# Kernel tuning notes

Measured on AMD Instinct MI355X. Metric: run time of the kernel, lower is better.

## Reference

```python
import jax, jax.numpy as jnp
import numpy as np

N, F_NODE, DIM, H, K, OUT, L = 200000, 16, 3, 128, 20, 4, 4


def setup_inputs() -> dict:
    key = jax.random.key(0)
    ks = jax.random.split(key, 10)
    x = jax.random.normal(ks[0], (N, F_NODE), jnp.float32)
    pos = jax.random.normal(ks[1], (N, DIM), jnp.float32)
    y = jax.random.normal(ks[2], (DIM,), jnp.float32)
    # eigenvector-like basis, roughly orthonormal columns scale
    phi = jax.random.normal(ks[3], (N, K), jnp.float32) / np.sqrt(N).astype(np.float32)
    # torch Linear convention: W is [out, in], y = x @ W.T + b
    lift_w = jax.random.normal(ks[4], (H, F_NODE + 2 * DIM), jnp.float32) * 0.05
    lift_b = jnp.zeros((H,), jnp.float32)
    lin_w = jax.random.normal(ks[5], (L, H, H), jnp.float32) * 0.05  # per-layer, bias=False
    kernel = jax.random.normal(ks[6], (L, K, H, H), jnp.float32) * 0.05
    lower_w = jax.random.normal(ks[7], (OUT, H), jnp.float32) * 0.05
    lower_b = jnp.zeros((OUT,), jnp.float32)
    return dict(x=x, pos=pos, y=y, phi=phi, lift_w=lift_w, lift_b=lift_b,
                lin_w=lin_w, kernel=kernel, lower_w=lower_w, lower_b=lower_b)


def reference(x, pos, y, phi, lift_w, lift_b, lin_w, kernel, lower_w, lower_b):
    # lift: concat node feats, positions, broadcast global y -> [N, F_NODE+2*DIM]
    h = jnp.concatenate([x, pos, y * jnp.ones_like(pos)], axis=1) @ lift_w.T + lift_b
    # pinv(phi) is identical every layer in the original; compute once. [K, N]
    phi_pinv = jnp.linalg.pinv(phi)
    for l in range(L):
        v = phi_pinv @ h                              # [K, H] spectral coefficients
        rv = jnp.einsum('kij,kj->ki', kernel[l], v)   # batched mode matvec (= nested vmap)
        h = jax.nn.elu(h @ lin_w[l].T + phi @ rv)     # [N, H]
    return h @ lower_w.T + lower_b                    # [N, OUT]
```

## Files before the change

kernel.cpp:

```cpp
#include <hip/hip_runtime.h>
#include <math.h>

#define Nn 200000
#define NT 3125

typedef __attribute__((ext_vector_type(8))) short short8;
typedef __attribute__((ext_vector_type(16))) float floatx16;

#define SWZ4(row, g) (((g) ^ ((row) & 7)) << 2)

__device__ __forceinline__ unsigned rnbf(float x) {
    unsigned u = __builtin_bit_cast(unsigned, x);
    return (u + 0x7fffu + ((u >> 16) & 1u)) >> 16;
}
__device__ __forceinline__ float asf(unsigned u) { return __builtin_bit_cast(float, u); }
__device__ __forceinline__ unsigned packf(float x) {
    unsigned hb = rnbf(x);
    float fh = asf(hb << 16);
    unsigned lb = rnbf(x - fh);
    return hb | (lb << 16);
}
__device__ __forceinline__ void permsplit(const unsigned* e, short8& hi, short8& lo) {
    uint4 h, l;
    h.x = __builtin_amdgcn_perm(e[1], e[0], 0x05040100u);
    h.y = __builtin_amdgcn_perm(e[3], e[2], 0x05040100u);
    h.z = __builtin_amdgcn_perm(e[5], e[4], 0x05040100u);
    h.w = __builtin_amdgcn_perm(e[7], e[6], 0x05040100u);
    l.x = __builtin_amdgcn_perm(e[1], e[0], 0x07060302u);
    l.y = __builtin_amdgcn_perm(e[3], e[2], 0x07060302u);
    l.z = __builtin_amdgcn_perm(e[5], e[4], 0x07060302u);
    l.w = __builtin_amdgcn_perm(e[7], e[6], 0x07060302u);
    hi = __builtin_bit_cast(short8, h);
    lo = __builtin_bit_cast(short8, l);
}
__device__ __forceinline__ void permsplit2(uint4 q0, uint4 q1, short8& hi, short8& lo) {
    unsigned e[8] = { q0.x, q0.y, q0.z, q0.w, q1.x, q1.y, q1.z, q1.w };
    permsplit(e, hi, lo);
}

__device__ __forceinline__ void pt_accum(const unsigned* As, const unsigned* Ph,
                                         float* __restrict__ PTc_blk, int t) {
    int lane = t & 63, w = t >> 6;
    int ln = lane & 31, hw = lane >> 5;
    int j0 = w * 32;
    floatx16 ap;
#pragma unroll
    for (int i = 0; i < 16; i++) ap[i] = 0.f;
#pragma unroll
    for (int ks = 0; ks < 4; ks++) {
        unsigned pa[8], e[8];
#pragma unroll
        for (int j = 0; j < 8; j++) {
            int node = ks * 16 + 8 * hw + j;
            pa[j] = Ph[node * 32 + SWZ4(node, ln >> 2) + (ln & 3)];
            int col = j0 + ln;
            e[j] = As[node * 128 + SWZ4(node, col >> 2) + (col & 3)];
        }
        short8 a_hi, a_lo, b_hi, b_lo;
        permsplit(pa, a_hi, a_lo);
        permsplit(e, b_hi, b_lo);
        ap = __builtin_amdgcn_mfma_f32_32x32x16_bf16(a_hi, b_hi, ap, 0, 0, 0);
        ap = __builtin_amdgcn_mfma_f32_32x32x16_bf16(a_lo, b_hi, ap, 0, 0, 0);
        ap = __builtin_amdgcn_mfma_f32_32x32x16_bf16(a_hi, b_lo, ap, 0, 0, 0);
    }
#pragma unroll
    for (int r = 0; r < 16; r++) {
        int mode = (r & 3) + 8 * (r >> 2) + 4 * hw;
        if (mode < 20) unsafeAtomicAdd(&PTc_blk[mode * 128 + j0 + ln], ap[r]);
    }
}

__device__ __forceinline__ void pt_mfma8(const unsigned* As, const unsigned* Ph,
                                         floatx16& ap, int t) {
    int lane = t & 63, w = t >> 6;
    int ln = lane & 31, hw = lane >> 5;
    int j0 = (w & 3) * 32;
    int nh = w >> 2;
#pragma unroll
    for (int i = 0; i < 16; i++) ap[i] = 0.f;
#pragma unroll
    for (int ks2 = 0; ks2 < 2; ks2++) {
        int ks = nh * 2 + ks2;
        unsigned pa[8], e[8];
#pragma unroll
        for (int j = 0; j < 8; j++) {
            int node = ks * 16 + 8 * hw + j;
            pa[j] = Ph[node * 32 + SWZ4(node, ln >> 2) + (ln & 3)];
            int col = j0 + ln;
            e[j] = As[node * 128 + SWZ4(node, col >> 2) + (col & 3)];
        }
        short8 a_hi, a_lo, b_hi, b_lo;
        permsplit(pa, a_hi, a_lo);
        permsplit(e, b_hi, b_lo);
        ap = __builtin_amdgcn_mfma_f32_32x32x16_bf16(a_hi, b_hi, ap, 0, 0, 0);
        ap = __builtin_amdgcn_mfma_f32_32x32x16_bf16(a_lo, b_hi, ap, 0, 0, 0);
        ap = __builtin_amdgcn_mfma_f32_32x32x16_bf16(a_hi, b_lo, ap, 0, 0, 0);
    }
}

__global__ void ptreduce_k(const float* __restrict__ PTc, float* __restrict__ PT) {
    int j = blockIdx.x * 128 + threadIdx.x;
    float s0 = 0.f, s1 = 0.f, s2 = 0.f, s3 = 0.f;
#pragma unroll
    for (int c = 0; c < 64; c += 4) {
        s0 += PTc[(size_t)c * 2560 + j];
        s1 += PTc[(size_t)(c + 1) * 2560 + j];
        s2 += PTc[(size_t)(c + 2) * 2560 + j];
        s3 += PTc[(size_t)(c + 3) * 2560 + j];
    }
    PT[j] = (s0 + s1) + (s2 + s3);
}

__global__ void bias_fold_k(const float* __restrict__ y, const float* __restrict__ lw,
                            const float* __restrict__ lb, float* __restrict__ b2) {
    int j = threadIdx.x;
    float s = lb[j];
#pragma unroll
    for (int d = 0; d < 3; d++) s += y[d] * lw[j * 22 + 19 + d];
    b2[j] = s;
}

__global__ void wsplit_k(const float* __restrict__ lw, const float* __restrict__ low_w,
                         unsigned short* __restrict__ Wh, unsigned short* __restrict__ Wl,
                         unsigned short* __restrict__ LWh, unsigned short* __restrict__ LWl) {
    int i = blockIdx.x * 256 + threadIdx.x;
    float w;
    unsigned short *ph, *pl;
    int idx;
    if (i < 65536) { w = lw[i]; ph = Wh; pl = Wl; idx = i; }
    else           { w = low_w[i - 65536]; ph = LWh; pl = LWl; idx = i - 65536; }
    unsigned hb = rnbf(w);
    float fh = asf(hb << 16);
    unsigned lb = rnbf(w - fh);
    ph[idx] = (unsigned short)hb;
    pl[idx] = (unsigned short)lb;
}

__global__ __launch_bounds__(256) void lift_k(const float* __restrict__ x,
                                              const float* __restrict__ pos,
                                              const float* __restrict__ phi,
                                              const float* __restrict__ lw,
                                              const float* __restrict__ b2,
                                              unsigned* __restrict__ hpk,
                                              float* __restrict__ PTc) {
    __shared__ union {
        struct { float xs[64][21]; float Wc[20][132]; } a;
        unsigned As[64 * 128];
    } sm;
    __shared__ unsigned Ph[64 * 32];
    int t = threadIdx.x;
    int n0 = blockIdx.x * 64;
    {
        int n = t >> 2, f4 = (t & 3) * 4;
        float4 xv = *(const float4*)(x + (size_t)(n0 + n) * 16 + f4);
        sm.a.xs[n][f4 + 0] = xv.x; sm.a.xs[n][f4 + 1] = xv.y;
        sm.a.xs[n][f4 + 2] = xv.z; sm.a.xs[n][f4 + 3] = xv.w;
    }
    if (t < 192) { int n = t / 3, d = t % 3; sm.a.xs[n][16 + d] = pos[(size_t)(n0 + n) * 3 + d]; }
    if (t < 64) sm.a.xs[t][19] = 1.f;
    for (int idx = t; idx < 2560; idx += 256) {
        int k = idx >> 7, j = idx & 127;
        sm.a.Wc[k][j] = (k < 19) ? lw[j * 22 + k] : b2[j];
    }
    for (int idx = t; idx < 2048; idx += 256) {
        int row = idx >> 5, kk = idx & 31;
        float pv = (kk < 20) ? phi[(size_t)(n0 + row) * 20 + kk] : 0.f;
        Ph[row * 32 + SWZ4(row, kk >> 2) + (kk & 3)] = packf(pv);
    }
    __syncthreads();
    int tx = t & 31, ty = t >> 5, i0 = tx * 4;
    float acc[8][4];
#pragma unroll
    for (int m = 0; m < 8; m++)
#pragma unroll
        for (int c = 0; c < 4; c++) acc[m][c] = 0.f;
#pragma unroll 4
    for (int k = 0; k < 20; k++) {
        float4 w = *(const float4*)&sm.a.Wc[k][i0];
#pragma unroll
        for (int m = 0; m < 8; m++) {
            float a = sm.a.xs[ty + 8 * m][k];
            acc[m][0] += a * w.x; acc[m][1] += a * w.y;
            acc[m][2] += a * w.z; acc[m][3] += a * w.w;
        }
    }
    __syncthreads();
#pragma unroll
    for (int m = 0; m < 8; m++) {
        uint4 o;
        o.x = packf(acc[m][0]); o.y = packf(acc[m][1]);
        o.z = packf(acc[m][2]); o.w = packf(acc[m][3]);
        int row = ty + 8 * m;
        *(uint4*)&hpk[(size_t)(n0 + row) * 128 + i0] = o;
        *(uint4*)&sm.As[row * 128 + SWZ4(row, tx)] = o;
    }
    __syncthreads();
    pt_accum(sm.As, Ph, PTc + (size_t)(blockIdx.x & 63) * 2560, t);
}

__global__ void gram_k(const float* __restrict__ phi, float* __restrict__ G) {
    __shared__ float ph[64 * 20];
    int t = threadIdx.x;
    int i0 = t / 20, j0 = t % 20;
    int p1 = t + 256;
    int i1 = p1 / 20, j1 = p1 % 20;
    float a0 = 0.f, a1 = 0.f;
    for (int tile = blockIdx.x; tile < NT; tile += gridDim.x) {
        const float* src = phi + tile * 1280;
        for (int idx = t; idx < 1280; idx += 256) ph[idx] = src[idx];
        __syncthreads();
        for (int n = 0; n < 64; n++) {
            const float* r = ph + n * 20;
            a0 += r[i0] * r[j0];
            if (p1 < 400) a1 += r[i1] * r[j1];
        }
        __syncthreads();
    }
    unsafeAtomicAdd(&G[t], a0);
    if (p1 < 400) unsafeAtomicAdd(&G[p1], a1);
}

__global__ void ginv_k(const float* __restrict__ G, float* __restrict__ Gi) {
    __shared__ float A[20][40];
    __shared__ float colp[20];
    __shared__ float piv;
    int t = threadIdx.x;
    for (int idx = t; idx < 400; idx += 64) {
        int r = idx / 20, c = idx % 20;
        A[r][c] = G[idx];
        A[r][c + 20] = (r == c) ? 1.f : 0.f;
    }
    __syncthreads();
    for (int p = 0; p < 20; p++) {
        if (t == 0) piv = 1.f / A[p][p];
        __syncthreads();
        for (int c = t; c < 40; c += 64) A[p][c] *= piv;
        __syncthreads();
        if (t < 20) colp[t] = A[t][p];
        __syncthreads();
        for (int e = t; e < 800; e += 64) {
            int r = e / 40, c = e % 40;
            if (r != p) A[r][c] -= colp[r] * A[p][c];
        }
        __syncthreads();
    }
    for (int idx = t; idx < 400; idx += 64) {
        int r = idx / 20, c = idx % 20;
        Gi[idx] = A[r][c + 20];
    }
}

__global__ void rv_k(const float* __restrict__ Gi, const float* __restrict__ PT,
                     const float* __restrict__ kern_l,
                     unsigned short* __restrict__ RVh, unsigned short* __restrict__ RVl) {
    __shared__ __align__(16) float v[128];
    __shared__ float part[128];
    int k = blockIdx.x;
    int t = threadIdx.x;
    if (t < 128) {
        const float* gr = Gi + k * 20;
        float s = 0.f;
#pragma unroll
        for (int m = 0; m < 20; m++) s += gr[m] * PT[m * 128 + t];
        v[t] = s;
    }
    __syncthreads();
    int i = t & 127, half = t >> 7;
    const float* kr = kern_l + (size_t)(k * 128 + i) * 128 + half * 64;
    const float* vk = v + half * 64;
    float acc = 0.f;
#pragma unroll 4
    for (int jj = 0; jj < 64; jj += 4) {
        float4 kv = *(const float4*)(kr + jj);
        float4 vv = *(const float4*)(vk + jj);
        acc += kv.x * vv.x + kv.y * vv.y + kv.z * vv.z + kv.w * vv.w;
    }
    if (half) part[i] = acc;
    __syncthreads();
    if (!half) {
        float rv = acc + part[i];
        unsigned hb = rnbf(rv);
        float fh = asf(hb << 16);
        unsigned lb = rnbf(rv - fh);
        RVh[i * 32 + k] = (unsigned short)hb;
        RVl[i * 32 + k] = (unsigned short)lb;
    }
}

__global__ __launch_bounds__(512, 8) void update_k(unsigned* __restrict__ hpk,
                                                   const float* __restrict__ phi,
                                                   const unsigned short* __restrict__ Wh,
                                                   const unsigned short* __restrict__ Wl,
                                                   const unsigned short* __restrict__ RVh,
                                                   const unsigned short* __restrict__ RVl,
                                                   float* __restrict__ ptn,
                                                   const unsigned short* __restrict__ LWh,
                                                   const unsigned short* __restrict__ LWl,
                                                   const float* __restrict__ low_b,
                                                   float* __restrict__ outp) {
    __shared__ __align__(16) unsigned As[64 * 128];
    __shared__ __align__(16) unsigned Ph[64 * 32];
    int t = threadIdx.x;
    int n0 = blockIdx.x * 64;
    for (int idx = t; idx < 2048; idx += 512) {
        int row = idx >> 5, g = idx & 31;
        uint4 v = *(const uint4*)(hpk + (size_t)(n0 + row) * 128 + g * 4);
        *(uint4*)&As[row * 128 + SWZ4(row, g)] = v;
    }
    for (int idx = t; idx < 2048; idx += 512) {
        int row = idx >> 5, kk = idx & 31;
        float pv = (kk < 20) ? phi[(size_t)(n0 + row) * 20 + kk] : 0.f;
        Ph[row * 32 + SWZ4(row, kk >> 2) + (kk & 3)] = packf(pv);
    }
    __syncthreads();

    int lane = t & 63, w = t >> 6;
    int ln = lane & 31, hw = lane >> 5;
    int r0 = (w >> 2) * 32, ct0 = (w & 3) * 32;
    int arow = r0 + ln;

    floatx16 acc;
#pragma unroll
    for (int i = 0; i < 16; i++) acc[i] = 0.f;

    const unsigned short* whp = Wh + (size_t)(ct0 + ln) * 128 + 8 * hw;
    const unsigned short* wlp = Wl + (size_t)(ct0 + ln) * 128 + 8 * hw;
    const unsigned* abase = As + arow * 128;

#pragma unroll
    for (int ks = 0; ks < 8; ks++) {
        int k0 = ks * 16;
        int ga = 4 * ks + 2 * hw;
        uint4 aq0 = *(const uint4*)(abase + SWZ4(arow, ga));
        uint4 aq1 = *(const uint4*)(abase + SWZ4(arow, ga + 1));
        uint4 wh = *(const uint4*)(whp + k0);
        uint4 wl = *(const uint4*)(wlp + k0);
        short8 a_hi, a_lo;
        permsplit2(aq0, aq1, a_hi, a_lo);
        short8 bh = __builtin_bit_cast(short8, wh);
        short8 bl = __builtin_bit_cast(short8, wl);
        acc = __builtin_amdgcn_mfma_f32_32x32x16_bf16(a_hi, bh, acc, 0, 0, 0);
        acc = __builtin_amdgcn_mfma_f32_32x32x16_bf16(a_lo, bh, acc, 0, 0, 0);
        acc = __builtin_amdgcn_mfma_f32_32x32x16_bf16(a_hi, bl, acc, 0, 0, 0);
    }

    const unsigned* pbase = Ph + arow * 32;
#pragma unroll
    for (int ks = 0; ks < 2; ks++) {
        int k0 = ks * 16;
        int gr = 4 * ks + 2 * hw;
        uint4 q0 = *(const uint4*)(pbase + SWZ4(arow, gr));
        uint4 q1 = *(const uint4*)(pbase + SWZ4(arow, gr + 1));
        short8 a_hi, a_lo;
        permsplit2(q0, q1, a_hi, a_lo);
        short8 bh = __builtin_bit_cast(short8, *(const uint4*)(RVh + (size_t)(ct0 + ln) * 32 + k0 + 8 * hw));
        short8 bl = __builtin_bit_cast(short8, *(const uint4*)(RVl + (size_t)(ct0 + ln) * 32 + k0 + 8 * hw));
        acc = __builtin_amdgcn_mfma_f32_32x32x16_bf16(a_hi, bh, acc, 0, 0, 0);
        acc = __builtin_amdgcn_mfma_f32_32x32x16_bf16(a_lo, bh, acc, 0, 0, 0);
        acc = __builtin_amdgcn_mfma_f32_32x32x16_bf16(a_hi, bl, acc, 0, 0, 0);
    }

    unsigned p0[16];
#pragma unroll
    for (int r = 0; r < 16; r++) {
        float v0 = acc[r];
        v0 = v0 > 0.f ? v0 : __expf(v0) - 1.f;
        p0[r] = packf(v0);
    }
    if (!outp) {
#pragma unroll
        for (int r = 0; r < 16; r++) {
            int row = (r & 3) + 8 * (r >> 2) + 4 * hw;
            hpk[(size_t)(n0 + r0 + row) * 128 + ct0 + ln] = p0[r];
        }
    }
    if (ptn || outp) {
        __syncthreads();
#pragma unroll
        for (int r = 0; r < 16; r++) {
            int row = r0 + (r & 3) + 8 * (r >> 2) + 4 * hw;
            int c0 = ct0 + ln;
            As[row * 128 + SWZ4(row, c0 >> 2) + (c0 & 3)] = p0[r];
        }
        __syncthreads();
        if (outp) {
            float* scr = (float*)Ph;
            int r0o = (w >> 1) * 32, kh = w & 1;
            int arow2 = r0o + ln;
            const unsigned* ab2 = As + arow2 * 128;
            floatx16 ap;
#pragma unroll
            for (int i = 0; i < 16; i++) ap[i] = 0.f;
            if (w < 4) {
#pragma unroll
                for (int kk = 0; kk < 4; kk++) {
                    int ks = kh * 4 + kk;
                    int ga = 4 * ks + 2 * hw;
                    uint4 q0 = *(const uint4*)(ab2 + SWZ4(arow2, ga));
                    uint4 q1 = *(const uint4*)(ab2 + SWZ4(arow2, ga + 1));
                    short8 a_hi, a_lo;
                    permsplit2(q0, q1, a_hi, a_lo);
                    short8 bh = { 0, 0, 0, 0, 0, 0, 0, 0 };
                    short8 bl = { 0, 0, 0, 0, 0, 0, 0, 0 };
                    if (ln < 4) {
                        bh = __builtin_bit_cast(short8, *(const uint4*)(LWh + ln * 128 + ks * 16 + 8 * hw));
                        bl = __builtin_bit_cast(short8, *(const uint4*)(LWl + ln * 128 + ks * 16 + 8 * hw));
                    }
                    ap = __builtin_amdgcn_mfma_f32_32x32x16_bf16(a_hi, bh, ap, 0, 0, 0);
                    ap = __builtin_amdgcn_mfma_f32_32x32x16_bf16(a_lo, bh, ap, 0, 0, 0);
                    ap = __builtin_amdgcn_mfma_f32_32x32x16_bf16(a_hi, bl, ap, 0, 0, 0);
                }
            }
            if (w < 4 && kh == 1 && ln < 4) {
#pragma unroll
                for (int r = 0; r < 16; r++) {
                    int row = (r & 3) + 8 * (r >> 2) + 4 * hw;
                    scr[(w >> 1) * 128 + row * 4 + ln] = ap[r];
                }
            }
            __syncthreads();
            if (w < 4 && kh == 0 && ln < 4) {
                float b = low_b[ln];
#pragma unroll
                for (int r = 0; r < 16; r++) {
                    int row = (r & 3) + 8 * (r >> 2) + 4 * hw;
                    float s = ap[r] + scr[(w >> 1) * 128 + row * 4 + ln] + b;
                    outp[(size_t)(n0 + r0o + row) * 4 + ln] = s;
                }
            }
        } else {
            floatx16 ap;
            pt_mfma8(As, Ph, ap, t);
            int j0 = (w & 3) * 32, nh = w >> 2;
            __syncthreads();
            float* PTs = (float*)As;
            if (nh == 1) {
#pragma unroll
                for (int r = 0; r < 16; r++) {
                    int mode = (r & 3) + 8 * (r >> 2) + 4 * hw;
                    if (mode < 20) PTs[mode * 128 + j0 + ln] = ap[r];
                }
            }
            __syncthreads();
            if (nh == 0) {
                float* blk = ptn + (size_t)(blockIdx.x & 63) * 2560;
#pragma unroll
                for (int r = 0; r < 16; r++) {
                    int mode = (r & 3) + 8 * (r >> 2) + 4 * hw;
                    if (mode < 20) {
                        int idx = mode * 128 + j0 + ln;
                        unsafeAtomicAdd(&blk[idx], ap[r] + PTs[idx]);
                    }
                }
            }
        }
    }
}

extern "C" void kernel_launch(void* const* d_in, const int* in_sizes, int n_in,
                              void* d_out, int out_size, void* d_ws, size_t ws_size,
                              hipStream_t stream) {
    (void)in_sizes; (void)n_in; (void)out_size; (void)ws_size;
    const float* x       = (const float*)d_in[0];
    const float* pos     = (const float*)d_in[1];
    const float* y       = (const float*)d_in[2];
    const float* phi     = (const float*)d_in[3];
    const float* lift_w  = (const float*)d_in[4];
    const float* lift_b  = (const float*)d_in[5];
    const float* lin_w   = (const float*)d_in[6];
    const float* kern    = (const float*)d_in[7];
    const float* lower_w = (const float*)d_in[8];
    const float* lower_b = (const float*)d_in[9];
    float* out = (float*)d_out;

    char* ws = (char*)d_ws;
    unsigned* hpk = (unsigned*)ws;
    size_t off = (size_t)Nn * 128 * 4;
    float* b2  = (float*)(ws + off);       off += 512;
    float* G   = (float*)(ws + off);       off += 1600;
    float* Gi  = (float*)(ws + off);       off += 1600;
    off = (off + 15) & ~(size_t)15;
    float* PT  = (float*)(ws + off);       off += 10240;
    float* PTc = (float*)(ws + off);       off += 64 * 2560 * 4;
    unsigned short* W_hi = (unsigned short*)(ws + off);  off += 131072;
    unsigned short* W_lo = (unsigned short*)(ws + off);  off += 131072;
    unsigned short* RVh  = (unsigned short*)(ws + off);  off += 8192;
    unsigned short* RVl  = (unsigned short*)(ws + off);  off += 8192;
    unsigned short* LWh  = (unsigned short*)(ws + off);  off += 1024;
    unsigned short* LWl  = (unsigned short*)(ws + off);  off += 1024;

    hipMemsetAsync(G, 0, 1600, stream);
    hipMemsetAsync(PTc, 0, 64 * 2560 * 4, stream);
    hipMemsetAsync(RVh, 0, 8192, stream);
    hipMemsetAsync(RVl, 0, 8192, stream);
    bias_fold_k<<<1, 128, 0, stream>>>(y, lift_w, lift_b, b2);
    wsplit_k<<<258, 256, 0, stream>>>(lin_w, lower_w, W_hi, W_lo, LWh, LWl);
    lift_k<<<NT, 256, 0, stream>>>(x, pos, phi, lift_w, b2, hpk, PTc);
    gram_k<<<256, 256, 0, stream>>>(phi, G);
    ginv_k<<<1, 64, 0, stream>>>(G, Gi);
    ptreduce_k<<<20, 128, 0, stream>>>(PTc, PT);

    for (int l = 0; l < 4; l++) {
        rv_k<<<20, 256, 0, stream>>>(Gi, PT, kern + (size_t)l * 20 * 128 * 128, RVh, RVl);
        float* ptc = (l < 3) ? PTc : (float*)nullptr;
        if (ptc) hipMemsetAsync(ptc, 0, 64 * 2560 * 4, stream);
        update_k<<<NT, 512, 0, stream>>>(hpk, phi, W_hi + (size_t)l * 16384,
                                         W_lo + (size_t)l * 16384, RVh, RVl, ptc,
                                         LWh, LWl, lower_b,
                                         (l == 3) ? out : (float*)nullptr);
        if (ptc) ptreduce_k<<<20, 128, 0, stream>>>(PTc, PT);
    }
}
```

Baseline: 616.4 us.

## Store split hi/lo bf16 planes in LDS, widen rv_k grid, fold bias into lift

The update kernel now stores activations and phi in LDS as separate hi and lo bf16 planes, so the MFMA inner loops read them directly instead of repacking with perm operations on every k-step. The PT accumulation now gathers 16-bit elements and packs them itself. rv_k is launched on a 2D grid with a shuffle reduction, which gives it more blocks. The bias_fold kernel and one memset are merged into lift_k and a single larger memset to cut launch count. The cost is extra 16-bit scalar LDS gathers in the PT path, and the 16-bit stores in the writeback may cause more bank conflicts.

```diff
diff --git a/kernel.cpp b/kernel.cpp
--- a/kernel.cpp
+++ b/kernel.cpp
@@ -33,10 +33,6 @@
     hi = __builtin_bit_cast(short8, h);
     lo = __builtin_bit_cast(short8, l);
 }
-__device__ __forceinline__ void permsplit2(uint4 q0, uint4 q1, short8& hi, short8& lo) {
-    unsigned e[8] = { q0.x, q0.y, q0.z, q0.w, q1.x, q1.y, q1.z, q1.w };
-    permsplit(e, hi, lo);
-}
 
 __device__ __forceinline__ void pt_accum(const unsigned* As, const unsigned* Ph,
                                          float* __restrict__ PTc_blk, int t) {
@@ -70,34 +66,6 @@
     }
 }
 
-__device__ __forceinline__ void pt_mfma8(const unsigned* As, const unsigned* Ph,
-                                         floatx16& ap, int t) {
-    int lane = t & 63, w = t >> 6;
-    int ln = lane & 31, hw = lane >> 5;
-    int j0 = (w & 3) * 32;
-    int nh = w >> 2;
-#pragma unroll
-    for (int i = 0; i < 16; i++) ap[i] = 0.f;
-#pragma unroll
-    for (int ks2 = 0; ks2 < 2; ks2++) {
-        int ks = nh * 2 + ks2;
-        unsigned pa[8], e[8];
-#pragma unroll
-        for (int j = 0; j < 8; j++) {
-            int node = ks * 16 + 8 * hw + j;
-            pa[j] = Ph[node * 32 + SWZ4(node, ln >> 2) + (ln & 3)];
-            int col = j0 + ln;
-            e[j] = As[node * 128 + SWZ4(node, col >> 2) + (col & 3)];
-        }
-        short8 a_hi, a_lo, b_hi, b_lo;
-        permsplit(pa, a_hi, a_lo);
-        permsplit(e, b_hi, b_lo);
-        ap = __builtin_amdgcn_mfma_f32_32x32x16_bf16(a_hi, b_hi, ap, 0, 0, 0);
-        ap = __builtin_amdgcn_mfma_f32_32x32x16_bf16(a_lo, b_hi, ap, 0, 0, 0);
-        ap = __builtin_amdgcn_mfma_f32_32x32x16_bf16(a_hi, b_lo, ap, 0, 0, 0);
-    }
-}
-
 __global__ void ptreduce_k(const float* __restrict__ PTc, float* __restrict__ PT) {
     int j = blockIdx.x * 128 + threadIdx.x;
     float s0 = 0.f, s1 = 0.f, s2 = 0.f, s3 = 0.f;
@@ -109,15 +77,6 @@
         s3 += PTc[(size_t)(c + 3) * 2560 + j];
     }
     PT[j] = (s0 + s1) + (s2 + s3);
-}
-
-__global__ void bias_fold_k(const float* __restrict__ y, const float* __restrict__ lw,
-                            const float* __restrict__ lb, float* __restrict__ b2) {
-    int j = threadIdx.x;
-    float s = lb[j];
-#pragma unroll
-    for (int d = 0; d < 3; d++) s += y[d] * lw[j * 22 + 19 + d];
-    b2[j] = s;
 }
 
 __global__ void wsplit_k(const float* __restrict__ lw, const float* __restrict__ low_w,
@@ -140,7 +99,8 @@
                                               const float* __restrict__ pos,
                                               const float* __restrict__ phi,
                                               const float* __restrict__ lw,
-                                              const float* __restrict__ b2,
+                                              const float* __restrict__ lb,
+                                              const float* __restrict__ yg,
                                               unsigned* __restrict__ hpk,
                                               float* __restrict__ PTc) {
     __shared__ union {
@@ -160,7 +120,14 @@
     if (t < 64) sm.a.xs[t][19] = 1.f;
     for (int idx = t; idx < 2560; idx += 256) {
         int k = idx >> 7, j = idx & 127;
-        sm.a.Wc[k][j] = (k < 19) ? lw[j * 22 + k] : b2[j];
+        float wv;
+        if (k < 19) {
+            wv = lw[j * 22 + k];
+        } else {
+            wv = lb[j] + yg[0] * lw[j * 22 + 19] + yg[1] * lw[j * 22 + 20]
+                       + yg[2] * lw[j * 22 + 21];
+        }
+        sm.a.Wc[k][j] = wv;
     }
     for (int idx = t; idx < 2048; idx += 256) {
         int row = idx >> 5, kk = idx & 31;
@@ -254,7 +221,6 @@
                      const float* __restrict__ kern_l,
                      unsigned short* __restrict__ RVh, unsigned short* __restrict__ RVl) {
     __shared__ __align__(16) float v[128];
-    __shared__ float part[128];
     int k = blockIdx.x;
     int t = threadIdx.x;
     if (t < 128) {
@@ -265,23 +231,24 @@
         v[t] = s;
     }
     __syncthreads();
-    int i = t & 127, half = t >> 7;
-    const float* kr = kern_l + (size_t)(k * 128 + i) * 128 + half * 64;
-    const float* vk = v + half * 64;
-    float acc = 0.f;
-#pragma unroll 4
-    for (int jj = 0; jj < 64; jj += 4) {
-        float4 kv = *(const float4*)(kr + jj);
-        float4 vv = *(const float4*)(vk + jj);
-        acc += kv.x * vv.x + kv.y * vv.y + kv.z * vv.z + kv.w * vv.w;
-    }
-    if (half) part[i] = acc;
-    __syncthreads();
-    if (!half) {
-        float rv = acc + part[i];
-        unsigned hb = rnbf(rv);
+    int il = t >> 4, seg = t & 15;
+    int i = blockIdx.y * 16 + il;
+    const float* kr = kern_l + (size_t)(k * 128 + i) * 128 + seg * 8;
+    const float* vk = v + seg * 8;
+    float4 ka = *(const float4*)kr;
+    float4 kb = *(const float4*)(kr + 4);
+    float4 va = *(const float4*)vk;
+    float4 vb = *(const float4*)(vk + 4);
+    float acc = ka.x * va.x + ka.y * va.y + ka.z * va.z + ka.w * va.w
+              + kb.x * vb.x + kb.y * vb.y + kb.z * vb.z + kb.w * vb.w;
+    acc += __shfl_xor(acc, 8);
+    acc += __shfl_xor(acc, 4);
+    acc += __shfl_xor(acc, 2);
+    acc += __shfl_xor(acc, 1);
+    if (seg == 0) {
+        unsigned hb = rnbf(acc);
         float fh = asf(hb << 16);
-        unsigned lb = rnbf(rv - fh);
+        unsigned lb = rnbf(acc - fh);
         RVh[i * 32 + k] = (unsigned short)hb;
         RVl[i * 32 + k] = (unsigned short)lb;
     }
@@ -298,19 +265,33 @@
                                                    const unsigned short* __restrict__ LWl,
                                                    const float* __restrict__ low_b,
                                                    float* __restrict__ outp) {
-    __shared__ __align__(16) unsigned As[64 * 128];
-    __shared__ __align__(16) unsigned Ph[64 * 32];
+    __shared__ __align__(16) unsigned short Ash[64 * 128];
+    __shared__ __align__(16) unsigned short Asl[64 * 128];
+    __shared__ __align__(16) unsigned short Phh[64 * 32];
+    __shared__ __align__(16) unsigned short Phl[64 * 32];
     int t = threadIdx.x;
     int n0 = blockIdx.x * 64;
     for (int idx = t; idx < 2048; idx += 512) {
         int row = idx >> 5, g = idx & 31;
         uint4 v = *(const uint4*)(hpk + (size_t)(n0 + row) * 128 + g * 4);
-        *(uint4*)&As[row * 128 + SWZ4(row, g)] = v;
+        uint2 hv, lv;
+        hv.x = __builtin_amdgcn_perm(v.y, v.x, 0x05040100u);
+        hv.y = __builtin_amdgcn_perm(v.w, v.z, 0x05040100u);
+        lv.x = __builtin_amdgcn_perm(v.y, v.x, 0x07060302u);
+        lv.y = __builtin_amdgcn_perm(v.w, v.z, 0x07060302u);
+        int base = row * 128 + (((g >> 1) ^ (row & 7)) << 3) + (g & 1) * 4;
+        *(uint2*)&Ash[base] = hv;
+        *(uint2*)&Asl[base] = lv;
     }
     for (int idx = t; idx < 2048; idx += 512) {
         int row = idx >> 5, kk = idx & 31;
         float pv = (kk < 20) ? phi[(size_t)(n0 + row) * 20 + kk] : 0.f;
-        Ph[row * 32 + SWZ4(row, kk >> 2) + (kk & 3)] = packf(pv);
+        unsigned hb = rnbf(pv);
+        float fh = asf(hb << 16);
+        unsigned lb = rnbf(pv - fh);
+        int pi = row * 32 + (((kk >> 3) ^ (row & 3)) << 3) + (kk & 7);
+        Phh[pi] = (unsigned short)hb;
+        Phl[pi] = (unsigned short)lb;
     }
     __syncthreads();
 
@@ -325,34 +306,32 @@
 
     const unsigned short* whp = Wh + (size_t)(ct0 + ln) * 128 + 8 * hw;
     const unsigned short* wlp = Wl + (size_t)(ct0 + ln) * 128 + 8 * hw;
-    const unsigned* abase = As + arow * 128;
+    const unsigned short* ahb = Ash + arow * 128;
+    const unsigned short* alb = Asl + arow * 128;
+    int r7 = arow & 7;
 
 #pragma unroll
     for (int ks = 0; ks < 8; ks++) {
         int k0 = ks * 16;
-        int ga = 4 * ks + 2 * hw;
-        uint4 aq0 = *(const uint4*)(abase + SWZ4(arow, ga));
-        uint4 aq1 = *(const uint4*)(abase + SWZ4(arow, ga + 1));
-        uint4 wh = *(const uint4*)(whp + k0);
-        uint4 wl = *(const uint4*)(wlp + k0);
-        short8 a_hi, a_lo;
-        permsplit2(aq0, aq1, a_hi, a_lo);
-        short8 bh = __builtin_bit_cast(short8, wh);
-        short8 bl = __builtin_bit_cast(short8, wl);
+        int gh = ((2 * ks + hw) ^ r7) << 3;
+        short8 a_hi = __builtin_bit_cast(short8, *(const uint4*)(ahb + gh));
+        short8 a_lo = __builtin_bit_cast(short8, *(const uint4*)(alb + gh));
+        short8 bh = __builtin_bit_cast(short8, *(const uint4*)(whp + k0));
+        short8 bl = __builtin_bit_cast(short8, *(const uint4*)(wlp + k0));
         acc = __builtin_amdgcn_mfma_f32_32x32x16_bf16(a_hi, bh, acc, 0, 0, 0);
         acc = __builtin_amdgcn_mfma_f32_32x32x16_bf16(a_lo, bh, acc, 0, 0, 0);
         acc = __builtin_amdgcn_mfma_f32_32x32x16_bf16(a_hi, bl, acc, 0, 0, 0);
     }
 
-    const unsigned* pbase = Ph + arow * 32;
+    const unsigned short* phb = Phh + arow * 32;
+    const unsigned short* plb = Phl + arow * 32;
+    int r3 = arow & 3;
 #pragma unroll
     for (int ks = 0; ks < 2; ks++) {
         int k0 = ks * 16;
-        int gr = 4 * ks + 2 * hw;
-        uint4 q0 = *(const uint4*)(pbase + SWZ4(arow, gr));
-        uint4 q1 = *(const uint4*)(pbase + SWZ4(arow, gr + 1));
-        short8 a_hi, a_lo;
-        permsplit2(q0, q1, a_hi, a_lo);
+        int gp = ((2 * ks + hw) ^ r3) << 3;
+        short8 a_hi = __builtin_bit_cast(short8, *(const uint4*)(phb + gp));
+        short8 a_lo = __builtin_bit_cast(short8, *(const uint4*)(plb + gp));
         short8 bh = __builtin_bit_cast(short8, *(const uint4*)(RVh + (size_t)(ct0 + ln) * 32 + k0 + 8 * hw));
         short8 bl = __builtin_bit_cast(short8, *(const uint4*)(RVl + (size_t)(ct0 + ln) * 32 + k0 + 8 * hw));
         acc = __builtin_amdgcn_mfma_f32_32x32x16_bf16(a_hi, bh, acc, 0, 0, 0);
@@ -380,14 +359,18 @@
         for (int r = 0; r < 16; r++) {
             int row = r0 + (r & 3) + 8 * (r >> 2) + 4 * hw;
             int c0 = ct0 + ln;
-            As[row * 128 + SWZ4(row, c0 >> 2) + (c0 & 3)] = p0[r];
+            int si = row * 128 + (((c0 >> 3) ^ (row & 7)) << 3) + (c0 & 7);
+            Ash[si] = (unsigned short)p0[r];
+            Asl[si] = (unsigned short)(p0[r] >> 16);
         }
         __syncthreads();
         if (outp) {
-            float* scr = (float*)Ph;
+            float* scr = (float*)Phh;
             int r0o = (w >> 1) * 32, kh = w & 1;
             int arow2 = r0o + ln;
-            const unsigned* ab2 = As + arow2 * 128;
+            const unsigned short* ah2 = Ash + arow2 * 128;
+            const unsigned short* al2 = Asl + arow2 * 128;
+            int rr7 = arow2 & 7;
             floatx16 ap;
 #pragma unroll
             for (int i = 0; i < 16; i++) ap[i] = 0.f;
@@ -395,11 +378,9 @@
 #pragma unroll
                 for (int kk = 0; kk < 4; kk++) {
                     int ks = kh * 4 + kk;
-                    int ga = 4 * ks + 2 * hw;
-                    uint4 q0 = *(const uint4*)(ab2 + SWZ4(arow2, ga));
-                    uint4 q1 = *(const uint4*)(ab2 + SWZ4(arow2, ga + 1));
-                    short8 a_hi, a_lo;
-                    permsplit2(q0, q1, a_hi, a_lo);
+                    int gh = ((2 * ks + hw) ^ rr7) << 3;
+                    short8 a_hi = __builtin_bit_cast(short8, *(const uint4*)(ah2 + gh));
+                    short8 a_lo = __builtin_bit_cast(short8, *(const uint4*)(al2 + gh));
                     short8 bh = { 0, 0, 0, 0, 0, 0, 0, 0 };
                     short8 bl = { 0, 0, 0, 0, 0, 0, 0, 0 };
                     if (ln < 4) {
@@ -429,11 +410,50 @@
                 }
             }
         } else {
+            int j0 = (w & 3) * 32, nh = w >> 2;
             floatx16 ap;
-            pt_mfma8(As, Ph, ap, t);
-            int j0 = (w & 3) * 32, nh = w >> 2;
+#pragma unroll
+            for (int i = 0; i < 16; i++) ap[i] = 0.f;
+#pragma unroll
+            for (int ks2 = 0; ks2 < 2; ks2++) {
+                int ks = nh * 2 + ks2;
+                unsigned short ah[8], al[8], bh[8], bl[8];
+#pragma unroll
+                for (int j = 0; j < 8; j++) {
+                    int node = ks * 16 + 8 * hw + j;
+                    int pi = node * 32 + (((ln >> 3) ^ (node & 3)) << 3) + (ln & 7);
+                    ah[j] = Phh[pi]; al[j] = Phl[pi];
+                    int col = j0 + ln;
+                    int si = node * 128 + (((col >> 3) ^ (node & 7)) << 3) + (col & 7);
+                    bh[j] = Ash[si]; bl[j] = Asl[si];
+                }
+                uint4 qa, qb, qc, qd;
+                qa.x = (unsigned)ah[0] | ((unsigned)ah[1] << 16);
+                qa.y = (unsigned)ah[2] | ((unsigned)ah[3] << 16);
+                qa.z = (unsigned)ah[4] | ((unsigned)ah[5] << 16);
+                qa.w = (unsigned)ah[6] | ((unsigned)ah[7] << 16);
+                qb.x = (unsigned)al[0] | ((unsigned)al[1] << 16);
+                qb.y = (unsigned)al[2] | ((unsigned)al[3] << 16);
+                qb.z = (unsigned)al[4] | ((unsigned)al[5] << 16);
+                qb.w = (unsigned)al[6] | ((unsigned)al[7] << 16);
+                qc.x = (unsigned)bh[0] | ((unsigned)bh[1] << 16);
+                qc.y = (unsigned)bh[2] | ((unsigned)bh[3] << 16);
+                qc.z = (unsigned)bh[4] | ((unsigned)bh[5] << 16);
+                qc.w = (unsigned)bh[6] | ((unsigned)bh[7] << 16);
+                qd.x = (unsigned)bl[0] | ((unsigned)bl[1] << 16);
+                qd.y = (unsigned)bl[2] | ((unsigned)bl[3] << 16);
+                qd.z = (unsigned)bl[4] | ((unsigned)bl[5] << 16);
+                qd.w = (unsigned)bl[6] | ((unsigned)bl[7] << 16);
+                short8 a_hi = __builtin_bit_cast(short8, qa);
+                short8 a_lo = __builtin_bit_cast(short8, qb);
+                short8 b_hi = __builtin_bit_cast(short8, qc);
+                short8 b_lo = __builtin_bit_cast(short8, qd);
+                ap = __builtin_amdgcn_mfma_f32_32x32x16_bf16(a_hi, b_hi, ap, 0, 0, 0);
+                ap = __builtin_amdgcn_mfma_f32_32x32x16_bf16(a_lo, b_hi, ap, 0, 0, 0);
+                ap = __builtin_amdgcn_mfma_f32_32x32x16_bf16(a_hi, b_lo, ap, 0, 0, 0);
+            }
             __syncthreads();
-            float* PTs = (float*)As;
+            float* PTs = (float*)Ash;
             if (nh == 1) {
 #pragma unroll
                 for (int r = 0; r < 16; r++) {
@@ -488,20 +508,20 @@
     unsigned short* RVl  = (unsigned short*)(ws + off);  off += 8192;
     unsigned short* LWh  = (unsigned short*)(ws + off);  off += 1024;
     unsigned short* LWl  = (unsigned short*)(ws + off);  off += 1024;
+    (void)b2;
 
     hipMemsetAsync(G, 0, 1600, stream);
     hipMemsetAsync(PTc, 0, 64 * 2560 * 4, stream);
-    hipMemsetAsync(RVh, 0, 8192, stream);
-    hipMemsetAsync(RVl, 0, 8192, stream);
-    bias_fold_k<<<1, 128, 0, stream>>>(y, lift_w, lift_b, b2);
+    hipMemsetAsync(RVh, 0, 16384, stream);
     wsplit_k<<<258, 256, 0, stream>>>(lin_w, lower_w, W_hi, W_lo, LWh, LWl);
-    lift_k<<<NT, 256, 0, stream>>>(x, pos, phi, lift_w, b2, hpk, PTc);
+    lift_k<<<NT, 256, 0, stream>>>(x, pos, phi, lift_w, lift_b, y, hpk, PTc);
     gram_k<<<256, 256, 0, stream>>>(phi, G);
     ginv_k<<<1, 64, 0, stream>>>(G, Gi);
     ptreduce_k<<<20, 128, 0, stream>>>(PTc, PT);
 
     for (int l = 0; l < 4; l++) {
-        rv_k<<<20, 256, 0, stream>>>(Gi, PT, kern + (size_t)l * 20 * 128 * 128, RVh, RVl);
+        rv_k<<<dim3(20, 8), 256, 0, stream>>>(Gi, PT, kern + (size_t)l * 20 * 128 * 128,
+                                              RVh, RVl);
         float* ptc = (l < 3) ? PTc : (float*)nullptr;
         if (ptc) hipMemsetAsync(ptc, 0, 64 * 2560 * 4, stream);
         update_k<<<NT, 512, 0, stream>>>(hpk, phi, W_hi + (size_t)l * 16384,
```

Result: no change. 605.2 us (-1.8%).
